# Kernel tuning notes

Measured on AMD Instinct MI355X. Metric: run time of the kernel, lower is better.

Reference implementation:

```python
import jax, jax.numpy as jnp
import numpy as np

U = 200000      # unique nodes
B = 20000       # node_list batch size
K = 33          # n_nbr_samples + self
F = 256         # feature_dim
E = 128         # emb_dim
BN_EPS = 1e-5


def setup_inputs() -> dict:
    key = jax.random.key(0)
    k1, k2, k3, k4 = jax.random.split(key, 4)
    return {
        "features": jax.random.normal(k1, (U, F), dtype=jnp.float32),
        "W": jax.random.normal(k2, (F, E), dtype=jnp.float32) * 0.05,
        "b": jax.random.normal(k3, (E,), dtype=jnp.float32) * 0.01,
        "gamma": jnp.ones((E,), dtype=jnp.float32),
        "beta": jnp.zeros((E,), dtype=jnp.float32),
        "sample_idx": jax.random.randint(k4, (B, K), 0, U, dtype=jnp.int64)
        if jax.config.jax_enable_x64 else jax.random.randint(k4, (B, K), 0, U, dtype=jnp.int32),
    }


def reference(features, W, b, gamma, beta, sample_idx):
    # fc: Linear -> BatchNorm1d (training-mode batch stats) -> Tanh; Dropout in eval (identity)
    h = features @ W + b                       # [U, E]
    mu = jnp.mean(h, axis=0)                   # [E]
    var = jnp.var(h, axis=0)                   # biased var, as torch BN uses for normalization
    h = jnp.tanh(gamma * (h - mu) * jax.lax.rsqrt(var + BN_EPS) + beta)  # [U, E]
    # Row-normalized 0/1 mask matmul == mean over the K distinct sampled unique-node rows
    gathered = h[sample_idx]                   # [B, K, E] irregular gather
    return jnp.mean(gathered, axis=1)          # [B, E]
```

## Files before the change

kernel.cpp:

```cpp
#include <hip/hip_runtime.h>

#define U_NODES 200000
#define B_ROWS  20000
#define K_S     33
#define F_DIM   256
#define E_DIM   128
#define NBLK    1563

typedef __bf16 bf16x8 __attribute__((ext_vector_type(8)));
typedef float  f32x4  __attribute__((ext_vector_type(4)));
typedef unsigned short ushortx4 __attribute__((ext_vector_type(4)));
typedef unsigned short ushortx8 __attribute__((ext_vector_type(8)));

__device__ __forceinline__ unsigned short f2bf(float f) {
    unsigned int u = __builtin_bit_cast(unsigned int, f);
    u += 0x7fffu + ((u >> 16) & 1u);
    return (unsigned short)(u >> 16);
}
__device__ __forceinline__ float bf2f(unsigned short s) {
    return __builtin_bit_cast(float, ((unsigned int)s) << 16);
}
__device__ __forceinline__ bf16x8 pack_bf8(f32x4 a, f32x4 b) {
    ushortx8 r;
    r[0] = f2bf(a[0]); r[1] = f2bf(a[1]); r[2] = f2bf(a[2]); r[3] = f2bf(a[3]);
    r[4] = f2bf(b[0]); r[5] = f2bf(b[1]); r[6] = f2bf(b[2]); r[7] = f2bf(b[3]);
    return __builtin_bit_cast(bf16x8, r);
}

__global__ void wprep_kernel(const float* __restrict__ W, unsigned short* __restrict__ Wt) {
    int n = blockIdx.x;
    int k = threadIdx.x;
    Wt[n * F_DIM + k] = f2bf(W[(size_t)k * E_DIM + n]);
}

__global__ __launch_bounds__(256) void gemm_stats_kernel(
    const float* __restrict__ A, const unsigned short* __restrict__ Wt,
    unsigned short* __restrict__ h, float* __restrict__ partial)
{
    __shared__ __attribute__((aligned(16))) char smem[65536];
    char* Ws = smem;

    const int t    = threadIdx.x;
    const int lane = t & 63;
    const int wv   = t >> 6;
    const int m    = lane & 15;
    const int qd   = lane >> 4;
    const int row0 = blockIdx.x * 128;

    int gr0 = row0 + wv * 32 + m;       if (gr0 >= U_NODES) gr0 = U_NODES - 1;
    int gr1 = row0 + wv * 32 + 16 + m;  if (gr1 >= U_NODES) gr1 = U_NODES - 1;
    const float* pa0 = A + (size_t)gr0 * F_DIM + qd * 8;
    const float* pa1 = A + (size_t)gr1 * F_DIM + qd * 8;

#define LOAD_CHUNK(P, c) do {                                                  \
        P[0] = *(const f32x4*)(pa0 + (c) * 64);                                \
        P[1] = *(const f32x4*)(pa0 + (c) * 64 + 4);                            \
        P[2] = *(const f32x4*)(pa0 + (c) * 64 + 32);                           \
        P[3] = *(const f32x4*)(pa0 + (c) * 64 + 36);                           \
        P[4] = *(const f32x4*)(pa1 + (c) * 64);                                \
        P[5] = *(const f32x4*)(pa1 + (c) * 64 + 4);                            \
        P[6] = *(const f32x4*)(pa1 + (c) * 64 + 32);                           \
        P[7] = *(const f32x4*)(pa1 + (c) * 64 + 36);                           \
    } while (0)

#define COMPUTE_CHUNK(P, c) do {                                               \
        bf16x8 a00 = pack_bf8(P[0], P[1]);                                     \
        bf16x8 a01 = pack_bf8(P[2], P[3]);                                     \
        bf16x8 a10 = pack_bf8(P[4], P[5]);                                     \
        bf16x8 a11 = pack_bf8(P[6], P[7]);                                     \
        _Pragma("unroll")                                                      \
        for (int ct = 0; ct < 8; ++ct) {                                       \
            int rb = ct * 16 + m;                                              \
            bf16x8 b0 = *(const bf16x8*)(Ws + rb * 512 +                       \
                            ((((c) * 8 + qd) ^ (rb & 7)) << 4));               \
            acc0[ct] = __builtin_amdgcn_mfma_f32_16x16x32_bf16(a00, b0, acc0[ct], 0, 0, 0); \
            acc1[ct] = __builtin_amdgcn_mfma_f32_16x16x32_bf16(a10, b0, acc1[ct], 0, 0, 0); \
            bf16x8 b1 = *(const bf16x8*)(Ws + rb * 512 +                       \
                            ((((c) * 8 + 4 + qd) ^ (rb & 7)) << 4));           \
            acc0[ct] = __builtin_amdgcn_mfma_f32_16x16x32_bf16(a01, b1, acc0[ct], 0, 0, 0); \
            acc1[ct] = __builtin_amdgcn_mfma_f32_16x16x32_bf16(a11, b1, acc1[ct], 0, 0, 0); \
        }                                                                      \
    } while (0)

    f32x4 pA[8], pB[8], pC[8], pD[8];
    LOAD_CHUNK(pA, 0);
    LOAD_CHUNK(pB, 1);
    LOAD_CHUNK(pC, 2);
    LOAD_CHUNK(pD, 3);

    #pragma unroll
    for (int i = 0; i < 16; ++i) {
        int flat = t + 256 * i;
        int r = flat >> 5, q = flat & 31;
        ushortx8 v = *(const ushortx8*)(Wt + (size_t)r * F_DIM + q * 8);
        *(ushortx8*)(Ws + r * 512 + ((q ^ (r & 7)) << 4)) = v;
    }

    f32x4 acc0[8], acc1[8];
    #pragma unroll
    for (int ct = 0; ct < 8; ++ct) {
        acc0[ct] = (f32x4){0.f, 0.f, 0.f, 0.f};
        acc1[ct] = (f32x4){0.f, 0.f, 0.f, 0.f};
    }

    __syncthreads();

    COMPUTE_CHUNK(pA, 0);
    COMPUTE_CHUNK(pB, 1);
    COMPUTE_CHUNK(pC, 2);
    COMPUTE_CHUNK(pD, 3);

#undef LOAD_CHUNK
#undef COMPUTE_CHUNK

    __syncthreads();

    const bool full = (row0 + 128) <= U_NODES;
    float s[8], sq[8];
    #pragma unroll
    for (int ct = 0; ct < 8; ++ct) {
        float ss = 0.f, qq = 0.f;
        #pragma unroll
        for (int v = 0; v < 4; ++v) {
            float x0 = acc0[ct][v];
            float x1 = acc1[ct][v];
            if (full || (row0 + wv * 32 + qd * 4 + v) < U_NODES)      { ss += x0; qq += x0 * x0; }
            if (full || (row0 + wv * 32 + 16 + qd * 4 + v) < U_NODES) { ss += x1; qq += x1 * x1; }
        }
        s[ct] = ss; sq[ct] = qq;
    }
    float* redS = (float*)smem;
    float* redQ = (float*)(smem + 8192);
    int rq = wv * 4 + qd;
    #pragma unroll
    for (int ct = 0; ct < 8; ++ct) {
        redS[rq * 128 + ct * 16 + m] = s[ct];
        redQ[rq * 128 + ct * 16 + m] = sq[ct];
    }
    __syncthreads();
    {
        float tot = 0.f;
        if (t < 128) {
            #pragma unroll
            for (int i = 0; i < 16; ++i) tot += redS[i * 128 + t];
        } else {
            #pragma unroll
            for (int i = 0; i < 16; ++i) tot += redQ[i * 128 + (t - 128)];
        }
        partial[(size_t)blockIdx.x * 256 + t] = tot;
    }
    __syncthreads();

    unsigned short* tb = (unsigned short*)(smem + wv * 8192);
    #pragma unroll
    for (int ct = 0; ct < 8; ++ct)
        #pragma unroll
        for (int v = 0; v < 4; ++v) {
            tb[(qd * 4 + v) * 128 + ct * 16 + m]        = f2bf(acc0[ct][v]);
            tb[(16 + qd * 4 + v) * 128 + ct * 16 + m]   = f2bf(acc1[ct][v]);
        }
    __syncthreads();
    #pragma unroll
    for (int i = 0; i < 8; ++i) {
        int idx = lane + 64 * i;
        int r = idx >> 4, c8 = (idx & 15) * 8;
        int gr = row0 + wv * 32 + r;
        if (gr < U_NODES)
            *(ushortx8*)(h + (size_t)gr * E_DIM + c8) = *(const ushortx8*)(tb + r * 128 + c8);
    }
}

__global__ __launch_bounds__(256) void reduce_finalize_kernel(
    const float* __restrict__ partial,
    const float* __restrict__ gamma, const float* __restrict__ beta,
    float* __restrict__ scale, float* __restrict__ shift)
{
    __shared__ float redS[256], redQ[256];
    const int c = blockIdx.x;
    const int t = threadIdx.x;
    float a = 0.f, b = 0.f;
    for (int j = t; j < NBLK; j += 256) {
        a += partial[(size_t)j * 256 + c];
        b += partial[(size_t)j * 256 + c + 128];
    }
    redS[t] = a; redQ[t] = b;
    __syncthreads();
    #pragma unroll
    for (int s = 128; s > 0; s >>= 1) {
        if (t < s) { redS[t] += redS[t + s]; redQ[t] += redQ[t + s]; }
        __syncthreads();
    }
    if (t == 0) {
        float mu  = redS[0] * (1.f / U_NODES);
        float var = redQ[0] * (1.f / U_NODES) - mu * mu;
        float inv = rsqrtf(var + 1e-5f);
        float sc  = gamma[c] * inv;
        scale[c] = sc;
        shift[c] = beta[c] - sc * mu;
    }
}

__global__ __launch_bounds__(256) void gather_kernel(
    const unsigned short* __restrict__ h, const int* __restrict__ sidx_g,
    const float* __restrict__ scale, const float* __restrict__ shift,
    float* __restrict__ out)
{
    __shared__ int sl[16 * K_S];
    const int t  = threadIdx.x;
    const int g  = t & 15;
    const int r  = t >> 4;
    const int b0 = blockIdx.x * 16;
    for (int i = t; i < 16 * K_S; i += 256) sl[i] = sidx_g[(size_t)b0 * K_S + i];
    float scv[8], shv[8];
    *(float4*)&scv[0] = *(const float4*)(scale + g * 8);
    *(float4*)&scv[4] = *(const float4*)(scale + g * 8 + 4);
    *(float4*)&shv[0] = *(const float4*)(shift + g * 8);
    *(float4*)&shv[4] = *(const float4*)(shift + g * 8 + 4);
    __syncthreads();

    float acc[8] = {0.f, 0.f, 0.f, 0.f, 0.f, 0.f, 0.f, 0.f};
    #pragma unroll
    for (int k = 0; k < K_S; ++k) {
        int idx = sl[r * K_S + k];
        ushortx8 v = *(const ushortx8*)(h + (size_t)idx * E_DIM + g * 8);
        #pragma unroll
        for (int j = 0; j < 8; ++j) {
            float x  = bf2f(v[j]) * scv[j] + shv[j];
            float ex = __expf(2.f * x);
            acc[j] += 1.f - 2.f * __builtin_amdgcn_rcpf(ex + 1.f);
        }
    }
    float* op = out + (size_t)(b0 + r) * E_DIM + g * 8;
    *(float4*)(op)     = make_float4(acc[0] * (1.f / K_S), acc[1] * (1.f / K_S),
                                     acc[2] * (1.f / K_S), acc[3] * (1.f / K_S));
    *(float4*)(op + 4) = make_float4(acc[4] * (1.f / K_S), acc[5] * (1.f / K_S),
                                     acc[6] * (1.f / K_S), acc[7] * (1.f / K_S));
}

extern "C" void kernel_launch(void* const* d_in, const int* in_sizes, int n_in,
                              void* d_out, int out_size, void* d_ws, size_t ws_size,
                              hipStream_t stream) {
    const float* features = (const float*)d_in[0];
    const float* W        = (const float*)d_in[1];
    const float* gamma    = (const float*)d_in[3];
    const float* beta     = (const float*)d_in[4];
    const int*   sample   = (const int*)d_in[5];
    float* out = (float*)d_out;

    float* scale   = (float*)d_ws;
    float* shift   = scale + 128;
    float* partial = shift + 128;
    unsigned short* Wt = (unsigned short*)(partial + (size_t)NBLK * 256);
    unsigned short* h  = Wt + 128 * 256;

    wprep_kernel<<<128, 256, 0, stream>>>(W, Wt);
    gemm_stats_kernel<<<NBLK, 256, 0, stream>>>(features, Wt, h, partial);
    reduce_finalize_kernel<<<128, 256, 0, stream>>>(partial, gamma, beta, scale, shift);
    gather_kernel<<<B_ROWS / 16, 256, 0, stream>>>(h, sample, scale, shift, out);
}
```

Before: 360.9 us.

## Stage A and W tiles through LDS with direct global-to-LDS loads

Replaces the register-prefetch of all four fp32 A chunks plus one full W copy into LDS with a K-loop over 64-wide slices. Each slice of A and W is loaded straight into swizzled LDS using global_load_lds, then read back for the MFMAs. This is meant to cut the number of live vector registers and to use the direct-to-LDS load path, which could raise occupancy. In exchange it adds two barriers per slice and exposes load latency, because nothing is double-buffered.

```diff
diff --git a/kernel.cpp b/kernel.cpp
--- a/kernel.cpp
+++ b/kernel.cpp
@@ -12,6 +12,9 @@
 typedef unsigned short ushortx4 __attribute__((ext_vector_type(4)));
 typedef unsigned short ushortx8 __attribute__((ext_vector_type(8)));
 
+typedef const __attribute__((address_space(1))) void* gptr_t;
+typedef __attribute__((address_space(3))) void* lptr_t;
+
 __device__ __forceinline__ unsigned short f2bf(float f) {
     unsigned int u = __builtin_bit_cast(unsigned int, f);
     u += 0x7fffu + ((u >> 16) & 1u);
@@ -37,8 +40,9 @@
     const float* __restrict__ A, const unsigned short* __restrict__ Wt,
     unsigned short* __restrict__ h, float* __restrict__ partial)
 {
-    __shared__ __attribute__((aligned(16))) char smem[65536];
-    char* Ws = smem;
+    __shared__ __attribute__((aligned(16))) char smem[49152];
+    char* As = smem;
+    char* Ws = smem + 32768;
 
     const int t    = threadIdx.x;
     const int lane = t & 63;
@@ -46,55 +50,10 @@
     const int m    = lane & 15;
     const int qd   = lane >> 4;
     const int row0 = blockIdx.x * 128;
-
-    int gr0 = row0 + wv * 32 + m;       if (gr0 >= U_NODES) gr0 = U_NODES - 1;
-    int gr1 = row0 + wv * 32 + 16 + m;  if (gr1 >= U_NODES) gr1 = U_NODES - 1;
-    const float* pa0 = A + (size_t)gr0 * F_DIM + qd * 8;
-    const float* pa1 = A + (size_t)gr1 * F_DIM + qd * 8;
-
-#define LOAD_CHUNK(P, c) do {                                                  \
-        P[0] = *(const f32x4*)(pa0 + (c) * 64);                                \
-        P[1] = *(const f32x4*)(pa0 + (c) * 64 + 4);                            \
-        P[2] = *(const f32x4*)(pa0 + (c) * 64 + 32);                           \
-        P[3] = *(const f32x4*)(pa0 + (c) * 64 + 36);                           \
-        P[4] = *(const f32x4*)(pa1 + (c) * 64);                                \
-        P[5] = *(const f32x4*)(pa1 + (c) * 64 + 4);                            \
-        P[6] = *(const f32x4*)(pa1 + (c) * 64 + 32);                           \
-        P[7] = *(const f32x4*)(pa1 + (c) * 64 + 36);                           \
-    } while (0)
-
-#define COMPUTE_CHUNK(P, c) do {                                               \
-        bf16x8 a00 = pack_bf8(P[0], P[1]);                                     \
-        bf16x8 a01 = pack_bf8(P[2], P[3]);                                     \
-        bf16x8 a10 = pack_bf8(P[4], P[5]);                                     \
-        bf16x8 a11 = pack_bf8(P[6], P[7]);                                     \
-        _Pragma("unroll")                                                      \
-        for (int ct = 0; ct < 8; ++ct) {                                       \
-            int rb = ct * 16 + m;                                              \
-            bf16x8 b0 = *(const bf16x8*)(Ws + rb * 512 +                       \
-                            ((((c) * 8 + qd) ^ (rb & 7)) << 4));               \
-            acc0[ct] = __builtin_amdgcn_mfma_f32_16x16x32_bf16(a00, b0, acc0[ct], 0, 0, 0); \
-            acc1[ct] = __builtin_amdgcn_mfma_f32_16x16x32_bf16(a10, b0, acc1[ct], 0, 0, 0); \
-            bf16x8 b1 = *(const bf16x8*)(Ws + rb * 512 +                       \
-                            ((((c) * 8 + 4 + qd) ^ (rb & 7)) << 4));           \
-            acc0[ct] = __builtin_amdgcn_mfma_f32_16x16x32_bf16(a01, b1, acc0[ct], 0, 0, 0); \
-            acc1[ct] = __builtin_amdgcn_mfma_f32_16x16x32_bf16(a11, b1, acc1[ct], 0, 0, 0); \
-        }                                                                      \
-    } while (0)
-
-    f32x4 pA[8], pB[8], pC[8], pD[8];
-    LOAD_CHUNK(pA, 0);
-    LOAD_CHUNK(pB, 1);
-    LOAD_CHUNK(pC, 2);
-    LOAD_CHUNK(pD, 3);
-
-    #pragma unroll
-    for (int i = 0; i < 16; ++i) {
-        int flat = t + 256 * i;
-        int r = flat >> 5, q = flat & 31;
-        ushortx8 v = *(const ushortx8*)(Wt + (size_t)r * F_DIM + q * 8);
-        *(ushortx8*)(Ws + r * 512 + ((q ^ (r & 7)) << 4)) = v;
-    }
+    const int wb   = t & 192;
+
+    const int r0 = wv * 32 + m;
+    const int r1 = r0 + 16;
 
     f32x4 acc0[8], acc1[8];
     #pragma unroll
@@ -103,17 +62,44 @@
         acc1[ct] = (f32x4){0.f, 0.f, 0.f, 0.f};
     }
 
-    __syncthreads();
-
-    COMPUTE_CHUNK(pA, 0);
-    COMPUTE_CHUNK(pB, 1);
-    COMPUTE_CHUNK(pC, 2);
-    COMPUTE_CHUNK(pD, 3);
-
-#undef LOAD_CHUNK
-#undef COMPUTE_CHUNK
-
-    __syncthreads();
+    for (int kk = 0; kk < F_DIM; kk += 64) {
+        #pragma unroll
+        for (int i = 0; i < 8; ++i) {
+            int S   = i * 256 + t;
+            int row = S >> 4, sl = S & 15;
+            int gr  = row0 + row; if (gr >= U_NODES) gr = U_NODES - 1;
+            const float* gsrc = A + (size_t)gr * F_DIM + kk + ((sl ^ (row & 15)) << 2);
+            __builtin_amdgcn_global_load_lds(
+                (gptr_t)gsrc, (lptr_t)(As + ((i * 256 + wb) << 4)), 16, 0, 0);
+        }
+        #pragma unroll
+        for (int i = 0; i < 4; ++i) {
+            int S   = i * 256 + t;
+            int row = S >> 3, sl = S & 7;
+            const unsigned short* gsrc = Wt + (size_t)row * F_DIM + kk + ((sl ^ (row & 7)) << 3);
+            __builtin_amdgcn_global_load_lds(
+                (gptr_t)gsrc, (lptr_t)(Ws + ((i * 256 + wb) << 4)), 16, 0, 0);
+        }
+        __syncthreads();
+
+        #pragma unroll
+        for (int hh = 0; hh < 2; ++hh) {
+            f32x4 a0lo = *(const f32x4*)(As + r0 * 256 + (((hh * 8 + qd * 2)     ^ (r0 & 15)) << 4));
+            f32x4 a0hi = *(const f32x4*)(As + r0 * 256 + (((hh * 8 + qd * 2 + 1) ^ (r0 & 15)) << 4));
+            f32x4 a1lo = *(const f32x4*)(As + r1 * 256 + (((hh * 8 + qd * 2)     ^ (r1 & 15)) << 4));
+            f32x4 a1hi = *(const f32x4*)(As + r1 * 256 + (((hh * 8 + qd * 2 + 1) ^ (r1 & 15)) << 4));
+            bf16x8 a0 = pack_bf8(a0lo, a0hi);
+            bf16x8 a1 = pack_bf8(a1lo, a1hi);
+            #pragma unroll
+            for (int ct = 0; ct < 8; ++ct) {
+                int rb = ct * 16 + m;
+                bf16x8 b = *(const bf16x8*)(Ws + rb * 128 + (((hh * 4 + qd) ^ (rb & 7)) << 4));
+                acc0[ct] = __builtin_amdgcn_mfma_f32_16x16x32_bf16(a0, b, acc0[ct], 0, 0, 0);
+                acc1[ct] = __builtin_amdgcn_mfma_f32_16x16x32_bf16(a1, b, acc1[ct], 0, 0, 0);
+            }
+        }
+        __syncthreads();
+    }
 
     const bool full = (row0 + 128) <= U_NODES;
     float s[8], sq[8];
```

New measurement: 338.4 us. 6.2% less time.
